# Optimization experiments

Hardware: AMD Instinct MI355X
Metric: run time of the kernel (lower is better)

Reference implementation:

```python
import jax, jax.numpy as jnp
import numpy as np

N_NODES = 100000


def sage_conv(x, edge_index, W_l, W_r, b):
    # PyG SAGEConv (aggr='mean', root_weight=True):
    # out_i = (mean_{j in N(i)} x_j) @ W_l + x_i @ W_r + b
    src, dst = edge_index[0], edge_index[1]
    msgs = x[src]                                             # [E, F] gather
    summed = jax.ops.segment_sum(msgs, dst, num_segments=N_NODES)
    deg = jax.ops.segment_sum(jnp.ones((edge_index.shape[1],), x.dtype), dst,
                              num_segments=N_NODES)
    mean = summed / jnp.maximum(deg, 1.0)[:, None]            # [N, F]
    return mean @ W_l + x @ W_r + b


def setup_inputs() -> dict:
    key = jax.random.key(0)
    ks = jax.random.split(key, 12)
    F, H = 128, 128
    E = 1600000
    s = lambda k, shp, fan: jax.random.normal(k, shp, jnp.float32) / np.sqrt(fan)
    return {
        "x": jax.random.normal(ks[0], (N_NODES, F), jnp.float32),
        "edge_index": jax.random.randint(ks[1], (2, E), 0, N_NODES, jnp.int64),
        "W1_l": s(ks[2], (F, H), F), "W1_r": s(ks[3], (F, H), F),
        "b1": jnp.zeros((H,), jnp.float32),
        "W2_l": s(ks[4], (H, H), H), "W2_r": s(ks[5], (H, H), H),
        "b2": jnp.zeros((H,), jnp.float32),
        "W3_l": s(ks[6], (H, 1), H), "W3_r": s(ks[7], (H, 1), H),
        "b3": jnp.zeros((1,), jnp.float32),
    }


def reference(x, edge_index, W1_l, W1_r, b1, W2_l, W2_r, b2, W3_l, W3_r, b3):
    h = jax.nn.relu(sage_conv(x, edge_index, W1_l, W1_r, b1))
    h = jax.nn.relu(sage_conv(h, edge_index, W2_l, W2_r, b2))
    h = sage_conv(h, edge_index, W3_l, W3_r, b3)   # [N, 1]
    return h.mean(axis=1)                          # [N]
```

## Files before the change

### kernel.cpp

```cpp
#include <hip/hip_runtime.h>


#define NN 100000
#define NB 391
#define SLAB 5120

typedef short bf16x8 __attribute__((ext_vector_type(8)));
typedef float f32x4 __attribute__((ext_vector_type(4)));

static __device__ __forceinline__ float uaf(unsigned u) { return __uint_as_float(u); }
static __device__ __forceinline__ unsigned short f2bf(float f) {
  unsigned u = __float_as_uint(f);
  u += 0x7fffu + ((u >> 16) & 1u);
  return (unsigned short)(u >> 16);
}

__global__ __launch_bounds__(256) void k_prep(
    const int* __restrict__ src, const int* __restrict__ dst, int E, int SB,
    int* __restrict__ cursor, unsigned* __restrict__ pairs,
    const float* __restrict__ x, unsigned short* __restrict__ Zrm,
    const float* __restrict__ W1l, const float* __restrict__ W1r,
    const float* __restrict__ W2l, const float* __restrict__ W2r,
    unsigned short* __restrict__ wt1, unsigned short* __restrict__ wt2) {
  __shared__ int h[NB];
  __shared__ int rb[NB];
  const int b = blockIdx.x;
  const int tid = threadIdx.x;
  const int XB = NN * 16 / 256;

  if (b < SB) {
    for (int i = tid; i < NB; i += 256) h[i] = 0;
    __syncthreads();
    int s[8], d[8];
    const int base = b * 2048 + tid * 8;
    #pragma unroll
    for (int i = 0; i < 8; i++) {
      int g = base + i;
      bool ok = g < E;
      s[i] = ok ? src[g] : 0;
      d[i] = ok ? dst[g] : -1;
      if (ok) atomicAdd(&h[d[i] >> 8], 1);
    }
    __syncthreads();
    for (int i = tid; i < NB; i += 256) {
      rb[i] = h[i] ? atomicAdd(&cursor[i], h[i]) : 0;
      h[i] = 0;
    }
    __syncthreads();
    #pragma unroll
    for (int i = 0; i < 8; i++) {
      if (d[i] >= 0) {
        int bk = d[i] >> 8;
        int off = rb[bk] + atomicAdd(&h[bk], 1);
        if (off < SLAB)
          pairs[(size_t)bk * SLAB + off] =
              ((unsigned)(d[i] & 255) << 17) | (unsigned)s[i];
      }
    }
  } else if (b < SB + XB) {
    int t = (b - SB) * 256 + tid;
    int node = t >> 4, c = t & 15;
    const float4* xp = (const float4*)(x + (size_t)node * 128 + c * 8);
    float4 a = xp[0], bb = xp[1];
    float v[8] = {a.x, a.y, a.z, a.w, bb.x, bb.y, bb.z, bb.w};
    unsigned hh[8];
    #pragma unroll
    for (int i = 0; i < 8; i++) hh[i] = f2bf(v[i]);
    uint4 p;
    p.x = hh[0] | (hh[1] << 16); p.y = hh[2] | (hh[3] << 16);
    p.z = hh[4] | (hh[5] << 16); p.w = hh[6] | (hh[7] << 16);
    *(uint4*)(Zrm + (size_t)node * 128 + c * 8) = p;
  } else if (b < SB + XB + 64) {
    #pragma unroll
    for (int it = 0; it < 4; it++) {
      int t = (b - SB - XB) * 1024 + it * 256 + tid;
      int layer = t >> 15;
      int rem = t & 32767;
      int k = rem >> 7;
      int nn = rem & 127;
      const float* Wl = layer ? W2l : W1l;
      const float* Wr = layer ? W2r : W1r;
      float v = (k < 128) ? Wl[k * 128 + nn] : Wr[(k - 128) * 128 + nn];
      unsigned short hv = f2bf(v);
      const int frag = (nn >> 4) * 8 + (k >> 7) * 4 + ((k >> 5) & 3);
      const int lane = ((k >> 3) & 3) * 16 + (nn & 15);
      const int addr = frag * 512 + lane * 8 + (k & 7);
      (layer ? wt2 : wt1)[addr] = hv;
    }
  } else {
    unsigned* zr = (unsigned*)(Zrm + (size_t)NN * 128);
    if (tid < 64) zr[tid] = 0;
  }
}

__global__ __launch_bounds__(256) void k_build(const unsigned* __restrict__ pairs,
                                               const int* __restrict__ cursor,
                                               int* __restrict__ beg, int* __restrict__ deg,
                                               int* __restrict__ csr, int N) {
  __shared__ int cnt[256];
  __shared__ int sd[256];
  __shared__ int cur[256];
  const int b = blockIdx.x;
  const int tid = threadIdx.x;
  const size_t p0 = (size_t)b * SLAB;
  int count = cursor[b];
  if (count > SLAB) count = SLAB;
  cnt[tid] = 0;
  cur[tid] = 0;
  __syncthreads();
  for (int i = tid; i < count; i += 256) atomicAdd(&cnt[pairs[p0 + i] >> 17], 1);
  __syncthreads();
  int v = cnt[tid];
  sd[tid] = v;
  __syncthreads();
  #pragma unroll
  for (int off = 1; off < 256; off <<= 1) {
    int u = (tid >= off) ? sd[tid - off] : 0;
    __syncthreads();
    sd[tid] += u;
    __syncthreads();
  }
  const int node = b * 256 + tid;
  if (node < N) {
    beg[node] = (int)p0 + (sd[tid] - v);
    deg[node] = v;
  }
  __syncthreads();
  for (int i = tid; i < count; i += 256) {
    unsigned pv = pairs[p0 + i];
    int dl = pv >> 17;
    int pos = (sd[dl] - cnt[dl]) + atomicAdd(&cur[dl], 1);
    csr[p0 + pos] = pv & 0x1ffff;
  }
}

#define ACC8(v)                                   \
  acc[0] += uaf((v).x << 16);                     \
  acc[1] += uaf((v).x & 0xffff0000u);             \
  acc[2] += uaf((v).y << 16);                     \
  acc[3] += uaf((v).y & 0xffff0000u);             \
  acc[4] += uaf((v).z << 16);                     \
  acc[5] += uaf((v).z & 0xffff0000u);             \
  acc[6] += uaf((v).w << 16);                     \
  acc[7] += uaf((v).w & 0xffff0000u);

__global__ __launch_bounds__(256) void k_aggZ(const unsigned short* __restrict__ Zrm,
                                              unsigned short* __restrict__ Zagg,
                                              const int* __restrict__ begA,
                                              const int* __restrict__ degA,
                                              const int* __restrict__ csr, int n) {
  const int wid = (blockIdx.x * blockDim.x + threadIdx.x) >> 6;
  const int lane = threadIdx.x & 63;
  if (wid >= n) return;
  const int beg = begA[wid];
  const int d = degA[wid];
  const int g = lane >> 4, c = lane & 15;
  float acc[8] = {0.f, 0.f, 0.f, 0.f, 0.f, 0.f, 0.f, 0.f};

  for (int base = 0; base < d; base += 64) {
    int m = d - base;
    if (m > 64) m = 64;
    int idx = csr[beg + base + (lane < m ? lane : 0)];
    for (int k = 0; k < m; k += 32) {
      uint4 vA[4], vB[4];
      const bool hasB = (k + 16) < m;
      #pragma unroll
      for (int u = 0; u < 4; u++) {
        int kk = k + u * 4 + g;
        int j = __shfl(idx, kk & 63);
        j = (kk < m) ? j : NN;
        vA[u] = *(const uint4*)(Zrm + (size_t)j * 128 + c * 8);
      }
      if (hasB) {
        #pragma unroll
        for (int u = 0; u < 4; u++) {
          int kk = k + 16 + u * 4 + g;
          int j = __shfl(idx, kk & 63);
          j = (kk < m) ? j : NN;
          vB[u] = *(const uint4*)(Zrm + (size_t)j * 128 + c * 8);
        }
      }
      #pragma unroll
      for (int u = 0; u < 4; u++) { ACC8(vA[u]); }
      if (hasB) {
        #pragma unroll
        for (int u = 0; u < 4; u++) { ACC8(vB[u]); }
      }
    }
  }
  #pragma unroll
  for (int j = 0; j < 8; j++) {
    acc[j] += __shfl_xor(acc[j], 16);
    acc[j] += __shfl_xor(acc[j], 32);
  }
  const float inv = d > 0 ? 1.0f / (float)d : 0.f;
  if (g == 0) {
    unsigned h[8];
    #pragma unroll
    for (int j = 0; j < 8; j++) h[j] = f2bf(acc[j] * inv);
    uint4 p;
    p.x = h[0] | (h[1] << 16); p.y = h[2] | (h[3] << 16);
    p.z = h[4] | (h[5] << 16); p.w = h[6] | (h[7] << 16);
    *(uint4*)(Zagg + (size_t)wid * 128 + c * 8) = p;
  }
}

template <int MODE>
__global__ __launch_bounds__(256, 2) void k_sage2(
    const unsigned short* __restrict__ Zagg, const unsigned short* __restrict__ Zroot,
    const unsigned short* __restrict__ WT, const float* __restrict__ bias,
    unsigned short* __restrict__ Zout,
    const float* __restrict__ w3l, const float* __restrict__ w3r,
    float* __restrict__ s2, float* __restrict__ r2, int n) {
  __shared__ __align__(16) unsigned short tile[4][8192];
  const int tid = threadIdx.x;
  const int lane = tid & 63;
  const int w = tid >> 6;
  const int ln = lane & 15;
  const int r16 = lane >> 4;
  const int m0 = blockIdx.x * 256 + w * 64;
  char* T = (char*)tile[w];

  f32x4 acc[4][8];
  #pragma unroll
  for (int s = 0; s < 4; s++)
    #pragma unroll
    for (int cc = 0; cc < 8; cc++) {
      acc[s][cc][0] = 0.f; acc[s][cc][1] = 0.f;
      acc[s][cc][2] = 0.f; acc[s][cc][3] = 0.f;
    }

  #pragma unroll
  for (int kh = 0; kh < 2; kh++) {
    const unsigned short* zsrc = kh ? Zroot : Zagg;
    #pragma unroll
    for (int i = 0; i < 16; i++) {
      const int nl = i * 4 + r16;
      uint4 v = *(const uint4*)(zsrc + (size_t)(m0 + nl) * 128 + ln * 8);
      *(uint4*)(T + nl * 256 + ((ln * 16) ^ ((nl & 7) << 4))) = v;
    }
    bf16x8 a[4][4];
    #pragma unroll
    for (int ks = 0; ks < 4; ks++)
      #pragma unroll
      for (int s = 0; s < 4; s++) {
        const int nl = s * 16 + ln;
        a[s][ks] = *(const bf16x8*)(T + nl * 256 +
                                    ((ks * 64 + r16 * 16) ^ ((nl & 7) << 4)));
      }
    #pragma unroll
    for (int ks = 0; ks < 4; ks++) {
      #pragma unroll
      for (int cg = 0; cg < 4; cg++) {
        bf16x8 bh[2];
        #pragma unroll
        for (int j = 0; j < 2; j++) {
          const size_t o = (size_t)(((cg * 2 + j) * 8 + kh * 4 + ks) * 512 + lane * 8);
          bh[j] = *(const bf16x8*)(WT + o);
        }
        #pragma unroll
        for (int j = 0; j < 2; j++) {
          #pragma unroll
          for (int s = 0; s < 4; s++) {
            acc[s][cg * 2 + j] =
                __builtin_amdgcn_mfma_f32_16x16x32_bf16(bh[j], a[s][ks], acc[s][cg * 2 + j], 0, 0, 0);
          }
        }
      }
    }
  }

  if (MODE == 0) {
    float4 bv4[8];
    #pragma unroll
    for (int cc = 0; cc < 8; cc++) bv4[cc] = *(const float4*)(bias + cc * 16 + r16 * 4);
    #pragma unroll
    for (int s = 0; s < 4; s++) {
      const int node = m0 + s * 16 + ln;
      if (node < n) {
        unsigned short* op = Zout + (size_t)node * 128 + r16 * 4;
        #pragma unroll
        for (int cc = 0; cc < 8; cc++) {
          ushort4 hq;
          hq.x = f2bf(fmaxf(acc[s][cc][0] + bv4[cc].x, 0.f));
          hq.y = f2bf(fmaxf(acc[s][cc][1] + bv4[cc].y, 0.f));
          hq.z = f2bf(fmaxf(acc[s][cc][2] + bv4[cc].z, 0.f));
          hq.w = f2bf(fmaxf(acc[s][cc][3] + bv4[cc].w, 0.f));
          *(ushort4*)(op + cc * 16) = hq;
        }
      }
    }
  } else {
    float4 bv4[8], wl4[8], wr4[8];
    #pragma unroll
    for (int cc = 0; cc < 8; cc++) {
      bv4[cc] = *(const float4*)(bias + cc * 16 + r16 * 4);
      wl4[cc] = *(const float4*)(w3l + cc * 16 + r16 * 4);
      wr4[cc] = *(const float4*)(w3r + cc * 16 + r16 * 4);
    }
    #pragma unroll
    for (int s = 0; s < 4; s++) {
      float sl = 0.f, sr = 0.f;
      #pragma unroll
      for (int cc = 0; cc < 8; cc++) {
        float v0 = fmaxf(acc[s][cc][0] + bv4[cc].x, 0.f);
        float v1 = fmaxf(acc[s][cc][1] + bv4[cc].y, 0.f);
        float v2 = fmaxf(acc[s][cc][2] + bv4[cc].z, 0.f);
        float v3 = fmaxf(acc[s][cc][3] + bv4[cc].w, 0.f);
        sl += v0 * wl4[cc].x + v1 * wl4[cc].y + v2 * wl4[cc].z + v3 * wl4[cc].w;
        sr += v0 * wr4[cc].x + v1 * wr4[cc].y + v2 * wr4[cc].z + v3 * wr4[cc].w;
      }
      sl += __shfl_xor(sl, 16); sl += __shfl_xor(sl, 32);
      sr += __shfl_xor(sr, 16); sr += __shfl_xor(sr, 32);
      const int node = m0 + s * 16 + ln;
      if (r16 == 0 && node < n) {
        s2[node] = sl;
        r2[node] = sr;
      }
    }
  }
}

__global__ __launch_bounds__(256) void k_out3(const float* __restrict__ s2,
                                              const float* __restrict__ r2,
                                              const int* __restrict__ beg,
                                              const int* __restrict__ deg,
                                              const int* __restrict__ csr,
                                              const float* __restrict__ b3,
                                              float* __restrict__ out, int n) {
  int t = blockIdx.x * blockDim.x + threadIdx.x;
  int node = t >> 4;
  int ln = t & 15;
  if (node >= n) return;
  int bg = beg[node], d = deg[node];
  float s = 0.f;
  for (int i = ln; i < d; i += 16) s += s2[csr[bg + i]];
  s += __shfl_xor(s, 1); s += __shfl_xor(s, 2);
  s += __shfl_xor(s, 4); s += __shfl_xor(s, 8);
  if (ln == 0) out[node] = s / (d > 0 ? (float)d : 1.0f) + r2[node] + b3[0];
}

extern "C" void kernel_launch(void* const* d_in, const int* in_sizes, int n_in,
                              void* d_out, int out_size, void* d_ws, size_t ws_size,
                              hipStream_t stream) {
  const float* x   = (const float*)d_in[0];
  const int*   ei  = (const int*)d_in[1];
  const float* W1l = (const float*)d_in[2];
  const float* W1r = (const float*)d_in[3];
  const float* b1  = (const float*)d_in[4];
  const float* W2l = (const float*)d_in[5];
  const float* W2r = (const float*)d_in[6];
  const float* b2  = (const float*)d_in[7];
  const float* W3l = (const float*)d_in[8];
  const float* W3r = (const float*)d_in[9];
  const float* b3  = (const float*)d_in[10];
  float* out = (float*)d_out;

  const int N = NN;
  const int E = in_sizes[1] / 2;
  const int* src = ei;
  const int* dst = ei + E;

  char* ws = (char*)d_ws;
  size_t off = 0;
  auto alloc = [&](size_t bytes) -> char* {
    char* p = ws + off;
    off = (off + bytes + 255) & ~(size_t)255;
    return p;
  };
  int* cursor = (int*)alloc((NB + 1) * 4);
  unsigned* pairs = (unsigned*)alloc((size_t)NB * SLAB * 4);
  int* csr  = (int*)alloc(((size_t)NB * SLAB + 128) * 4);
  int* beg  = (int*)alloc((size_t)N * 4);
  int* deg  = (int*)alloc((size_t)N * 4);
  float* s2 = (float*)alloc((size_t)N * 4);
  float* r2 = (float*)alloc((size_t)N * 4);
  unsigned short* wt1 = (unsigned short*)alloc(128 * 256 * 2);
  unsigned short* wt2 = (unsigned short*)alloc(128 * 256 * 2);
  unsigned short* Zrm  = (unsigned short*)alloc((size_t)(N + 160) * 128 * 2);
  unsigned short* Zagg = (unsigned short*)alloc((size_t)(N + 160) * 128 * 2);

  hipMemsetAsync(cursor, 0, (NB + 1) * 4, stream);

  const int SB = (E + 2047) / 2048;
  const int XB = N * 16 / 256;
  k_prep<<<SB + XB + 64 + 1, 256, 0, stream>>>(
      src, dst, E, SB, cursor, pairs, x, Zrm,
      W1l, W1r, W2l, W2r, wt1, wt2);
  k_build<<<NB, 256, 0, stream>>>(pairs, cursor, beg, deg, csr, N);

  const int wb = (N * 64 + 255) / 256;
  const int sb = (N + 255) / 256;
  k_aggZ<<<wb, 256, 0, stream>>>(Zrm, Zagg, beg, deg, csr, N);
  k_sage2<0><<<sb, 256, 0, stream>>>(Zagg, Zrm, wt1, b1, Zrm,
                                     nullptr, nullptr, nullptr, nullptr, N);
  k_aggZ<<<wb, 256, 0, stream>>>(Zrm, Zagg, beg, deg, csr, N);
  k_sage2<1><<<sb, 256, 0, stream>>>(Zagg, Zrm, wt2, b2, nullptr,
                                     W3l, W3r, s2, r2, N);
  k_out3<<<(N * 16 + 255) / 256, 256, 0, stream>>>(s2, r2, beg, deg, csr, b3, out, N);
}
```

Before: 241.5 us.

## Stage weight fragments in LDS and halve per-wave activation tile

Reorders the bf16 weight fragment layout so each K-half (aggregated or root) is a contiguous 16K-element block. The dense SAGE kernel now loads that block cooperatively into shared memory and reads B fragments from LDS instead of global memory. The per-wave activation tile is processed in two 64-column halves so total shared memory stays the same. The goal is to cut repeated global/L2 weight loads per wave, at the cost of extra __syncthreads barriers and LDS traffic.

```diff
diff --git a/kernel.cpp b/kernel.cpp
--- a/kernel.cpp
+++ b/kernel.cpp
@@ -82,7 +82,7 @@
       const float* Wr = layer ? W2r : W1r;
       float v = (k < 128) ? Wl[k * 128 + nn] : Wr[(k - 128) * 128 + nn];
       unsigned short hv = f2bf(v);
-      const int frag = (nn >> 4) * 8 + (k >> 7) * 4 + ((k >> 5) & 3);
+      const int frag = (k >> 7) * 32 + (nn >> 4) * 4 + ((k >> 5) & 3);
       const int lane = ((k >> 3) & 3) * 16 + (nn & 15);
       const int addr = frag * 512 + lane * 8 + (k & 7);
       (layer ? wt2 : wt1)[addr] = hv;
@@ -212,7 +212,8 @@
     unsigned short* __restrict__ Zout,
     const float* __restrict__ w3l, const float* __restrict__ w3r,
     float* __restrict__ s2, float* __restrict__ r2, int n) {
-  __shared__ __align__(16) unsigned short tile[4][8192];
+  __shared__ __align__(16) unsigned short wlds[16384];
+  __shared__ __align__(16) unsigned short tile[4][4096];
   const int tid = threadIdx.x;
   const int lane = tid & 63;
   const int w = tid >> 6;
@@ -220,6 +221,8 @@
   const int r16 = lane >> 4;
   const int m0 = blockIdx.x * 256 + w * 64;
   char* T = (char*)tile[w];
+  const int srow = lane >> 3;
+  const int schk = lane & 7;
 
   f32x4 acc[4][8];
   #pragma unroll
@@ -233,37 +236,50 @@
   #pragma unroll
   for (int kh = 0; kh < 2; kh++) {
     const unsigned short* zsrc = kh ? Zroot : Zagg;
-    #pragma unroll
-    for (int i = 0; i < 16; i++) {
-      const int nl = i * 4 + r16;
-      uint4 v = *(const uint4*)(zsrc + (size_t)(m0 + nl) * 128 + ln * 8);
-      *(uint4*)(T + nl * 256 + ((ln * 16) ^ ((nl & 7) << 4))) = v;
-    }
-    bf16x8 a[4][4];
-    #pragma unroll
-    for (int ks = 0; ks < 4; ks++)
-      #pragma unroll
-      for (int s = 0; s < 4; s++) {
-        const int nl = s * 16 + ln;
-        a[s][ks] = *(const bf16x8*)(T + nl * 256 +
-                                    ((ks * 64 + r16 * 16) ^ ((nl & 7) << 4)));
-      }
-    #pragma unroll
-    for (int ks = 0; ks < 4; ks++) {
-      #pragma unroll
-      for (int cg = 0; cg < 4; cg++) {
-        bf16x8 bh[2];
+    __syncthreads();
+    {
+      const unsigned short* wsrc = WT + (size_t)kh * 16384;
+      #pragma unroll
+      for (int i = 0; i < 8; i++) {
+        const int t = i * 256 + tid;
+        *(uint4*)(wlds + (size_t)t * 8) = *(const uint4*)(wsrc + (size_t)t * 8);
+      }
+    }
+    __syncthreads();
+    #pragma unroll
+    for (int half = 0; half < 2; half++) {
+      #pragma unroll
+      for (int i = 0; i < 8; i++) {
+        const int rr = i * 8 + srow;
+        uint4 v = *(const uint4*)(zsrc + (size_t)(m0 + rr) * 128 + half * 64 + schk * 8);
+        *(uint4*)(T + rr * 128 + ((schk * 16) ^ ((rr & 7) << 4))) = v;
+      }
+      bf16x8 a[4][2];
+      #pragma unroll
+      for (int k2 = 0; k2 < 2; k2++)
         #pragma unroll
-        for (int j = 0; j < 2; j++) {
-          const size_t o = (size_t)(((cg * 2 + j) * 8 + kh * 4 + ks) * 512 + lane * 8);
-          bh[j] = *(const bf16x8*)(WT + o);
+        for (int s = 0; s < 4; s++) {
+          const int nl = s * 16 + ln;
+          a[s][k2] = *(const bf16x8*)(T + nl * 128 +
+                                      ((k2 * 64 + r16 * 16) ^ ((nl & 7) << 4)));
         }
+      #pragma unroll
+      for (int k2 = 0; k2 < 2; k2++) {
+        const int ks = half * 2 + k2;
         #pragma unroll
-        for (int j = 0; j < 2; j++) {
+        for (int cg = 0; cg < 4; cg++) {
+          bf16x8 bh[2];
           #pragma unroll
-          for (int s = 0; s < 4; s++) {
-            acc[s][cg * 2 + j] =
-                __builtin_amdgcn_mfma_f32_16x16x32_bf16(bh[j], a[s][ks], acc[s][cg * 2 + j], 0, 0, 0);
+          for (int j = 0; j < 2; j++)
+            bh[j] = *(const bf16x8*)(wlds +
+                     (size_t)(((cg * 2 + j) * 4 + ks) * 512 + lane * 8));
+          #pragma unroll
+          for (int j = 0; j < 2; j++) {
+            #pragma unroll
+            for (int s = 0; s < 4; s++) {
+              acc[s][cg * 2 + j] =
+                  __builtin_amdgcn_mfma_f32_16x16x32_bf16(bh[j], a[s][k2], acc[s][cg * 2 + j], 0, 0, 0);
+            }
           }
         }
       }
```

Result: faster. 221.2 us (-8.4%).
